# Kernel tuning notes

Measured on AMD Instinct MI355X. Metric: run time of the kernel, lower is better.

Reference implementation:

```python
import jax, jax.numpy as jnp
import numpy as np

WIN = 4
HEAD_DIM = 32
N_HEADS = 6
TYPE = 'SW'
SHIFT = WIN // 2  # window_size // 2


def _relation():
    # [P, P, 3] relative coordinate indices into the (2w-1)^3 bias table
    cord = np.array([[i, j, k] for i in range(WIN) for j in range(WIN) for k in range(WIN)])
    return cord[:, None, :] - cord[None, :, :] + WIN - 1


def _shift_mask(nw):
    # boolean mask [nw^3, P, P]; True -> -inf (cross-boundary pairs in shifted windows)
    p, s = WIN, WIN - SHIFT
    m = np.zeros((nw, nw, nw, p, p, p, p, p, p), dtype=bool)
    m[-1, :, :, :s, :, :, s:, :, :] = True
    m[-1, :, :, s:, :, :, :s, :, :] = True
    m[:, -1, :, :, :s, :, :, s:, :] = True
    m[:, -1, :, :, s:, :, :, :s, :] = True
    m[:, :, -1, :, :, :s, :, :, s:] = True
    m[:, :, -1, :, :, s:, :, :, :s] = True
    return m.reshape(nw ** 3, p ** 3, p ** 3)


def setup_inputs() -> dict:
    key = jax.random.key(0)
    ks = jax.random.split(key, 6)
    dim = N_HEADS * HEAD_DIM  # 192
    B, S = 2, 32
    x = jax.random.normal(ks[0], (B, S, S, S, dim), jnp.float32)
    W_qkv = jax.random.normal(ks[1], (dim, 3 * dim), jnp.float32) * 0.02
    b_qkv = jnp.zeros((3 * dim,), jnp.float32)
    rel_params = jax.random.normal(ks[2], (N_HEADS, 2 * WIN - 1, 2 * WIN - 1, 2 * WIN - 1), jnp.float32) * 0.02
    W_out = jax.random.normal(ks[3], (dim, dim), jnp.float32) * 0.02
    b_out = jnp.zeros((dim,), jnp.float32)
    return {"x": x, "W_qkv": W_qkv, "b_qkv": b_qkv, "rel_params": rel_params, "W_out": W_out, "b_out": b_out}


def reference(x, W_qkv, b_qkv, rel_params, W_out, b_out):
    B, H, Wd, D, C = x.shape
    p = WIN
    nw = H // p
    scale = HEAD_DIM ** -0.5
    if TYPE != 'W':
        x = jnp.roll(x, (-SHIFT, -SHIFT, -SHIFT), axis=(1, 2, 3))
    # window partition: [B, NW, P, C], NW = nw^3, P = p^3
    xw = x.reshape(B, nw, p, nw, p, nw, p, C).transpose(0, 1, 3, 5, 2, 4, 6, 7).reshape(B, nw ** 3, p ** 3, C)
    qkv = xw @ W_qkv + b_qkv  # [B, NW, P, 3C]
    qkv = qkv.reshape(B, nw ** 3, p ** 3, 3 * N_HEADS, HEAD_DIM).transpose(3, 0, 1, 2, 4)  # [3h, B, NW, P, d]
    q, k, v = qkv[:N_HEADS], qkv[N_HEADS:2 * N_HEADS], qkv[2 * N_HEADS:]
    sim = jnp.einsum('hbwpc,hbwqc->hbwpq', q, k) * scale
    rel = _relation()
    bias = rel_params[:, rel[:, :, 0], rel[:, :, 1], rel[:, :, 2]]  # [h, P, P]
    sim = sim + bias[:, None, None, :, :]
    if TYPE != 'W':
        mask = jnp.asarray(_shift_mask(nw))[None, None]  # [1,1,NW,P,P]
        sim = jnp.where(mask, -jnp.inf, sim)
    probs = jax.nn.softmax(sim, axis=-1)
    out = jnp.einsum('hbwpq,hbwqc->hbwpc', probs, v)
    out = out.transpose(1, 2, 3, 0, 4).reshape(B, nw ** 3, p ** 3, C)  # h b w p c -> b w p (h c)
    out = out @ W_out + b_out
    out = out.reshape(B, nw, nw, nw, p, p, p, C).transpose(0, 1, 4, 2, 5, 3, 6, 7).reshape(B, H, Wd, D, C)
    if TYPE != 'W':
        out = jnp.roll(out, (SHIFT, SHIFT, SHIFT), axis=(1, 2, 3))
    return out
```

## Files before the change

### kernel.cpp

```cpp
#include <hip/hip_runtime.h>

typedef short bf16x8 __attribute__((ext_vector_type(8)));
typedef float f32x4 __attribute__((ext_vector_type(4)));

#define MFMA16(a, b, c) __builtin_amdgcn_mfma_f32_16x16x32_bf16(a, b, c, 0, 0, 0)

__device__ __forceinline__ unsigned short f2bf(float f) {
    unsigned int u = __float_as_uint(f);
    u += 0x7FFFu + ((u >> 16) & 1u);
    return (unsigned short)(u >> 16);
}
__device__ __forceinline__ unsigned int f2bf2(float a, float b) {
    unsigned int ua = __float_as_uint(a);
    ua += 0x7FFFu + ((ua >> 16) & 1u);
    unsigned int ub = __float_as_uint(b);
    ub += 0x7FFFu + ((ub >> 16) & 1u);
    return (ua >> 16) | (ub & 0xFFFF0000u);
}
#define DPPADD(v, CTRL)                                                        \
    {                                                                          \
        int _t = __builtin_amdgcn_mov_dpp(__float_as_int(v), CTRL, 0xf, 0xf, true); \
        v += __int_as_float(_t);                                               \
    }

#define WQT_OFF 0
#define WOT_OFF 221184
#define BQ_OFF  294912
#define TBL_OFF 297216

__global__ void prep_kernel(const float* __restrict__ Wqkv,
                            const float* __restrict__ bqkv,
                            const float* __restrict__ Wout,
                            const float* __restrict__ rel,
                            unsigned short* __restrict__ WqT,
                            unsigned short* __restrict__ WoT,
                            float* __restrict__ bq,
                            float* __restrict__ tblB) {
    __shared__ float tile[32][33];
    const float LOG2E = 1.4426950408889634f;
    const float SCALE = 0.17677669529663687f * 1.4426950408889634f;
    int bid = blockIdx.x;
    int tx = threadIdx.x & 31, ty = threadIdx.x >> 5;
    if (bid < 108) {
        int tn = bid % 18, tc = bid / 18;
#pragma unroll
        for (int i = 0; i < 4; ++i)
            tile[ty + i * 8][tx] = Wqkv[(tc * 32 + ty + i * 8) * 576 + tn * 32 + tx];
        __syncthreads();
        bool isQ = (tn < 6);
#pragma unroll
        for (int i = 0; i < 4; ++i) {
            float v = tile[tx][ty + i * 8];
            if (isQ) v *= SCALE;
            WqT[(tn * 32 + ty + i * 8) * 192 + tc * 32 + tx] = f2bf(v);
        }
    } else if (bid < 144) {
        int bb = bid - 108;
        int tn = bb % 6, tc = bb / 6;
#pragma unroll
        for (int i = 0; i < 4; ++i)
            tile[ty + i * 8][tx] = Wout[(tc * 32 + ty + i * 8) * 192 + tn * 32 + tx];
        __syncthreads();
#pragma unroll
        for (int i = 0; i < 4; ++i)
            WoT[(tn * 32 + ty + i * 8) * 192 + tc * 32 + tx] = f2bf(tile[tx][ty + i * 8]);
    } else if (bid == 144) {
        for (int i = threadIdx.x; i < 576; i += 256) {
            float v = bqkv[i];
            if (i < 192) v *= SCALE;
            bq[i] = v;
        }
    } else {
        int e = (bid - 145) * 256 + threadIdx.x;
        int r = e & 3, f = (e >> 2) & 3;
        int lane = (e >> 4) & 63, mb = (e >> 10) & 3, h = e >> 12;
        int g = lane >> 4, l15 = lane & 15;
        int qy = l15 >> 2, qx = l15 & 3;
        int dz = mb - f + 3, dy = g - qy + 3, dx = r - qx + 3;
        tblB[e] = rel[((h * 7 + dz) * 7 + dy) * 7 + dx] * LOG2E;
    }
}

#define OFF_X   0
#define OFF_P   0
#define OFF_QK  12288
#define OFF_VT  37376
#define OFF_O   51200
#define SMEM_US 64512

__global__ __launch_bounds__(512) void wmsa_kernel(
    const float* __restrict__ x, const float* __restrict__ tblB,
    const float* __restrict__ bout,
    const unsigned short* __restrict__ WqT,
    const unsigned short* __restrict__ WoT,
    const float* __restrict__ bq, float* __restrict__ out) {
    __shared__ __align__(16) unsigned short smem[SMEM_US];

    const int tid = threadIdx.x;
    const int bw = blockIdx.x;
    const int b  = bw >> 9;
    const int w  = bw & 511;
    const int wz = w >> 6, wy = (w >> 3) & 7, wx = w & 7;

    const int lane = tid & 63;
    const int wv   = tid >> 6;
    const int g    = lane >> 4;
    const int l15  = lane & 15;

    {
        int t = tid >> 3, q8 = tid & 7;
        int tz = t >> 4, ty = (t >> 2) & 3, tx = t & 3;
        int gz = (wz * 4 + tz + 2) & 31;
        int gy = (wy * 4 + ty + 2) & 31;
        int gx = (wx * 4 + tx + 2) & 31;
        const float* xp = x + ((((b * 32 + gz) * 32 + gy) * 32 + gx)) * 192;
        int g0 = q8 >> 1, j0 = (q8 & 1) * 4, lt = t & 15;
#pragma unroll
        for (int k = 0; k < 6; ++k) {
            float4 v = *(const float4*)(xp + q8 * 4 + k * 32);
            uint2 pk;
            pk.x = f2bf2(v.x, v.y);
            pk.y = f2bf2(v.z, v.w);
            *(uint2*)&smem[OFF_X + ((((k * 4 + g0) * 4 + tz) * 16 + lt) * 8) + j0] = pk;
        }
    }

    int nb = wv;
    float bias = bq[nb * 16 + l15];
    bf16x8 bfr[6];
    {
        const unsigned short* wp = WqT + (nb * 16 + l15) * 192 + g * 8;
#pragma unroll
        for (int kk = 0; kk < 6; ++kk) bfr[kk] = *(const bf16x8*)(wp + kk * 32);
    }
    __syncthreads();

    {
        bf16x8 afr[4][6];
#pragma unroll
        for (int m = 0; m < 4; ++m)
#pragma unroll
            for (int kk = 0; kk < 6; ++kk)
                afr[m][kk] = *(const bf16x8*)&smem[OFF_X + (((kk * 4 + g) * 4 + m) * 16 + l15) * 8];

        while (true) {
            int nbN = nb + 8;
            bool more = (nbN < 36);
            bf16x8 bfrN[6];
            float biasN = 0.f;
            if (more) {
                biasN = bq[nbN * 16 + l15];
                const unsigned short* wp = WqT + (nbN * 16 + l15) * 192 + g * 8;
#pragma unroll
                for (int kk = 0; kk < 6; ++kk) bfrN[kk] = *(const bf16x8*)(wp + kk * 32);
            }
            int colg = nb * 16 + l15;
            bool isV = (nb >= 24);
#pragma unroll
            for (int m = 0; m < 4; ++m) {
                f32x4 acc = {bias, bias, bias, bias};
#pragma unroll
                for (int kk = 0; kk < 6; ++kk) acc = MFMA16(afr[m][kk], bfr[kk], acc);
                int row0 = m * 16 + g * 4;
                unsigned int u01 = f2bf2(acc[0], acc[1]);
                unsigned int u23 = f2bf2(acc[2], acc[3]);
                if (!isV) {
                    unsigned short* qk = &smem[OFF_QK + row0 * 392 + colg];
                    qk[0]    = (unsigned short)u01;
                    qk[392]  = (unsigned short)(u01 >> 16);
                    qk[784]  = (unsigned short)u23;
                    qk[1176] = (unsigned short)(u23 >> 16);
                } else {
                    uint2 pk; pk.x = u01; pk.y = u23;
                    *(uint2*)&smem[OFF_VT + (colg - 384) * 72 + row0] = pk;
                }
            }
            if (!more) break;
            nb = nbN;
            bias = biasN;
#pragma unroll
            for (int kk = 0; kk < 6; ++kk) bfr[kk] = bfrN[kk];
        }
    }
    __syncthreads();

    const bool sz = (wz == 7), sy = (wy == 7), sx = (wx == 7);
    const bool anym = sz | sy | sx;
    {
        const int qy = l15 >> 2, qx = l15 & 3;
        const bool my = sy && ((g < 2) != (qy < 2));
        bool mxr[4];
#pragma unroll
        for (int r = 0; r < 4; ++r) mxr[r] = sx && ((r < 2) != (qx < 2));
        unsigned short* pb = &smem[OFF_P + wv * 1152];
        const int it0 = wv * 3;
        int h = it0 >> 2, mb = it0 & 3;

        bf16x8 qf, kf[4];
        f32x4 bv[4];
        {
            const f32x4* tp = (const f32x4*)(tblB + ((h * 4 + mb) * 64 + lane) * 16);
#pragma unroll
            for (int f = 0; f < 4; ++f) bv[f] = tp[f];
            qf = *(const bf16x8*)&smem[OFF_QK + (mb * 16 + l15) * 392 + h * 32 + g * 8];
#pragma unroll
            for (int f = 0; f < 4; ++f)
                kf[f] = *(const bf16x8*)&smem[OFF_QK + (f * 16 + l15) * 392 + 192 + h * 32 + g * 8];
        }

#pragma unroll
        for (int ii = 0; ii < 3; ++ii) {
            bf16x8 qfN, kfN[4];
            f32x4 bvN[4];
            if (ii < 2) {
                int itN = it0 + ii + 1;
                int hN = itN >> 2, mbN = itN & 3;
                const f32x4* tp = (const f32x4*)(tblB + ((hN * 4 + mbN) * 64 + lane) * 16);
#pragma unroll
                for (int f = 0; f < 4; ++f) bvN[f] = tp[f];
                qfN = *(const bf16x8*)&smem[OFF_QK + (mbN * 16 + l15) * 392 + hN * 32 + g * 8];
#pragma unroll
                for (int f = 0; f < 4; ++f)
                    kfN[f] = *(const bf16x8*)&smem[OFF_QK + (f * 16 + l15) * 392 + 192 + hN * 32 + g * 8];
            }
            const int vtb = OFF_VT + (h * 32 + l15) * 72 + g * 8;
            bf16x8 v00 = *(const bf16x8*)&smem[vtb];
            bf16x8 v01 = *(const bf16x8*)&smem[vtb + 32];
            bf16x8 v10 = *(const bf16x8*)&smem[vtb + 16 * 72];
            bf16x8 v11 = *(const bf16x8*)&smem[vtb + 16 * 72 + 32];

            f32x4 s[4];
#pragma unroll
            for (int f = 0; f < 4; ++f) {
                f32x4 z = {0.f, 0.f, 0.f, 0.f};
                s[f] = MFMA16(qf, kf[f], z);
            }
            if (!anym) {
#pragma unroll
                for (int f = 0; f < 4; ++f)
#pragma unroll
                    for (int r = 0; r < 4; ++r)
                        s[f][r] = exp2f(s[f][r] + bv[f][r]);
            } else {
#pragma unroll
                for (int f = 0; f < 4; ++f) {
                    bool mzy = (sz && ((mb < 2) != (f < 2))) | my;
#pragma unroll
                    for (int r = 0; r < 4; ++r) {
                        float v = s[f][r] + bv[f][r];
                        v = (mzy | mxr[r]) ? -1e30f : v;
                        s[f][r] = exp2f(v);
                    }
                }
            }
            float inv[4];
#pragma unroll
            for (int r = 0; r < 4; ++r) {
                float sm = (s[0][r] + s[1][r]) + (s[2][r] + s[3][r]);
                DPPADD(sm, 0xB1);
                DPPADD(sm, 0x4E);
                DPPADD(sm, 0x124);
                DPPADD(sm, 0x128);
                inv[r] = __builtin_amdgcn_rcpf(sm);
            }
#pragma unroll
            for (int f = 0; f < 4; ++f) {
                unsigned int u01 = f2bf2(s[f][0], s[f][1]);
                unsigned int u23 = f2bf2(s[f][2], s[f][3]);
                unsigned short* pw = &pb[(g * 4) * 72 + f * 16 + l15];
                pw[0]   = (unsigned short)u01;
                pw[72]  = (unsigned short)(u01 >> 16);
                pw[144] = (unsigned short)u23;
                pw[216] = (unsigned short)(u23 >> 16);
            }
            bf16x8 pf0 = *(const bf16x8*)&pb[l15 * 72 + g * 8];
            bf16x8 pf1 = *(const bf16x8*)&pb[l15 * 72 + 32 + g * 8];
            f32x4 o0 = {0.f, 0.f, 0.f, 0.f}, o1 = {0.f, 0.f, 0.f, 0.f};
            o0 = MFMA16(pf0, v00, o0);
            o1 = MFMA16(pf0, v10, o1);
            o0 = MFMA16(pf1, v01, o0);
            o1 = MFMA16(pf1, v11, o1);
#pragma unroll
            for (int r = 0; r < 4; ++r) { o0[r] *= inv[r]; o1[r] *= inv[r]; }
            unsigned int a0 = f2bf2(o0[0], o0[1]), a1 = f2bf2(o0[2], o0[3]);
            unsigned int c0 = f2bf2(o1[0], o1[1]), c1 = f2bf2(o1[2], o1[3]);
            unsigned short* ow = &smem[OFF_O + (mb * 16 + g * 4) * 208 + h * 32 + l15];
            ow[0]        = (unsigned short)a0;
            ow[208]      = (unsigned short)(a0 >> 16);
            ow[416]      = (unsigned short)a1;
            ow[624]      = (unsigned short)(a1 >> 16);
            ow[16]       = (unsigned short)c0;
            ow[16 + 208] = (unsigned short)(c0 >> 16);
            ow[16 + 416] = (unsigned short)c1;
            ow[16 + 624] = (unsigned short)(c1 >> 16);
            if (ii < 2) {
                int itN = it0 + ii + 1;
                h = itN >> 2; mb = itN & 3;
                qf = qfN;
#pragma unroll
                for (int f = 0; f < 4; ++f) { kf[f] = kfN[f]; bv[f] = bvN[f]; }
            }
        }
    }

    const int mw = wv >> 2, nq = wv & 3;
    int col0 = nq * 16 + l15;
    float boc = bout[col0];
    bf16x8 bfr3[6];
    {
        const unsigned short* wp = WoT + col0 * 192 + g * 8;
#pragma unroll
        for (int kk = 0; kk < 6; ++kk) bfr3[kk] = *(const bf16x8*)(wp + kk * 32);
    }
    __syncthreads();

    {
        bf16x8 ofr[2][6];
#pragma unroll
        for (int mi = 0; mi < 2; ++mi)
#pragma unroll
            for (int kk = 0; kk < 6; ++kk)
                ofr[mi][kk] = *(const bf16x8*)&smem[OFF_O + ((mw * 2 + mi) * 16 + l15) * 208 + kk * 32 + g * 8];
#pragma unroll
        for (int nbi = 0; nbi < 3; ++nbi) {
            int col = (nq + nbi * 4) * 16 + l15;
            float boN = 0.f;
            bf16x8 bfrN[6];
            if (nbi < 2) {
                int colN = (nq + (nbi + 1) * 4) * 16 + l15;
                boN = bout[colN];
                const unsigned short* wp = WoT + colN * 192 + g * 8;
#pragma unroll
                for (int kk = 0; kk < 6; ++kk) bfrN[kk] = *(const bf16x8*)(wp + kk * 32);
            }
#pragma unroll
            for (int mi = 0; mi < 2; ++mi) {
                f32x4 acc = {boc, boc, boc, boc};
#pragma unroll
                for (int kk = 0; kk < 6; ++kk) acc = MFMA16(ofr[mi][kk], bfr3[kk], acc);
                int m = mw * 2 + mi;
                int gz = (wz * 4 + m + 2) & 31;
                int gy = (wy * 4 + g + 2) & 31;
#pragma unroll
                for (int r = 0; r < 4; ++r) {
                    int gx = (wx * 4 + r + 2) & 31;
                    out[(((b * 32 + gz) * 32 + gy) * 32 + gx) * 192 + col] = acc[r];
                }
            }
            boc = boN;
#pragma unroll
            for (int kk = 0; kk < 6; ++kk) bfr3[kk] = bfrN[kk];
        }
    }
}

extern "C" void kernel_launch(void* const* d_in, const int* in_sizes, int n_in,
                              void* d_out, int out_size, void* d_ws, size_t ws_size,
                              hipStream_t stream) {
    const float* x    = (const float*)d_in[0];
    const float* Wqkv = (const float*)d_in[1];
    const float* bqkv = (const float*)d_in[2];
    const float* rel  = (const float*)d_in[3];
    const float* Wout = (const float*)d_in[4];
    const float* bout = (const float*)d_in[5];

    unsigned short* WqT = (unsigned short*)((char*)d_ws + WQT_OFF);
    unsigned short* WoT = (unsigned short*)((char*)d_ws + WOT_OFF);
    float*          bq  = (float*)((char*)d_ws + BQ_OFF);
    float*          tbl = (float*)((char*)d_ws + TBL_OFF);
    float*          out = (float*)d_out;

    prep_kernel<<<241, 256, 0, stream>>>(Wqkv, bqkv, Wout, rel, WqT, WoT, bq, tbl);
    wmsa_kernel<<<1024, 512, 0, stream>>>(x, tbl, bout, WqT, WoT, bq, out);
}
```

Before: 163.2 us.

## Double block size to 1024 threads and redistribute work across 16 waves

Raises the block from 8 to 16 wavefronts and splits every stage across them. The QKV projection now gives each wave half the rows, attention uses one or two head/row-block iterations per wave, and the output projection gives each wave one row block. An extra shared-memory region holds the additional waves' probability buffers. The intent is more latency hiding and parallelism per window, at the cost of more LDS per block, fewer resident blocks per CU, and uneven work across waves in the attention stage.

New measurement: 191.4 us. +17.3%, slower.

```diff
diff --git a/kernel.cpp b/kernel.cpp
--- a/kernel.cpp
+++ b/kernel.cpp
@@ -86,9 +86,10 @@
 #define OFF_QK  12288
 #define OFF_VT  37376
 #define OFF_O   51200
-#define SMEM_US 64512
-
-__global__ __launch_bounds__(512) void wmsa_kernel(
+#define OFF_P2  64512
+#define SMEM_US 71424
+
+__global__ __launch_bounds__(1024) void wmsa_kernel(
     const float* __restrict__ x, const float* __restrict__ tblB,
     const float* __restrict__ bout,
     const unsigned short* __restrict__ WqT,
@@ -108,24 +109,26 @@
     const int l15  = lane & 15;
 
     {
-        int t = tid >> 3, q8 = tid & 7;
+        int t = tid >> 4, q16 = tid & 15;
         int tz = t >> 4, ty = (t >> 2) & 3, tx = t & 3;
         int gz = (wz * 4 + tz + 2) & 31;
         int gy = (wy * 4 + ty + 2) & 31;
         int gx = (wx * 4 + tx + 2) & 31;
         const float* xp = x + ((((b * 32 + gz) * 32 + gy) * 32 + gx)) * 192;
-        int g0 = q8 >> 1, j0 = (q8 & 1) * 4, lt = t & 15;
-#pragma unroll
-        for (int k = 0; k < 6; ++k) {
-            float4 v = *(const float4*)(xp + q8 * 4 + k * 32);
+        int g0 = (q16 >> 1) & 3, j0 = (q16 & 1) * 4, k0 = q16 >> 3, lt = t & 15;
+#pragma unroll
+        for (int k = 0; k < 3; ++k) {
+            float4 v = *(const float4*)(xp + q16 * 4 + k * 64);
             uint2 pk;
             pk.x = f2bf2(v.x, v.y);
             pk.y = f2bf2(v.z, v.w);
-            *(uint2*)&smem[OFF_X + ((((k * 4 + g0) * 4 + tz) * 16 + lt) * 8) + j0] = pk;
-        }
-    }
-
-    int nb = wv;
+            int kk = k0 + 2 * k;
+            *(uint2*)&smem[OFF_X + ((((kk * 4 + g0) * 4 + tz) * 16 + lt) * 8) + j0] = pk;
+        }
+    }
+
+    int nb = wv >> 1;
+    const int mh2 = (wv & 1) * 2;
     float bias = bq[nb * 16 + l15];
     bf16x8 bfr[6];
     {
@@ -136,12 +139,12 @@
     __syncthreads();
 
     {
-        bf16x8 afr[4][6];
-#pragma unroll
-        for (int m = 0; m < 4; ++m)
+        bf16x8 afr[2][6];
+#pragma unroll
+        for (int mi = 0; mi < 2; ++mi)
 #pragma unroll
             for (int kk = 0; kk < 6; ++kk)
-                afr[m][kk] = *(const bf16x8*)&smem[OFF_X + (((kk * 4 + g) * 4 + m) * 16 + l15) * 8];
+                afr[mi][kk] = *(const bf16x8*)&smem[OFF_X + (((kk * 4 + g) * 4 + (mh2 + mi)) * 16 + l15) * 8];
 
         while (true) {
             int nbN = nb + 8;
@@ -157,11 +160,11 @@
             int colg = nb * 16 + l15;
             bool isV = (nb >= 24);
 #pragma unroll
-            for (int m = 0; m < 4; ++m) {
+            for (int mi = 0; mi < 2; ++mi) {
                 f32x4 acc = {bias, bias, bias, bias};
 #pragma unroll
-                for (int kk = 0; kk < 6; ++kk) acc = MFMA16(afr[m][kk], bfr[kk], acc);
-                int row0 = m * 16 + g * 4;
+                for (int kk = 0; kk < 6; ++kk) acc = MFMA16(afr[mi][kk], bfr[kk], acc);
+                int row0 = (mh2 + mi) * 16 + g * 4;
                 unsigned int u01 = f2bf2(acc[0], acc[1]);
                 unsigned int u23 = f2bf2(acc[2], acc[3]);
                 if (!isV) {
@@ -192,9 +195,9 @@
         bool mxr[4];
 #pragma unroll
         for (int r = 0; r < 4; ++r) mxr[r] = sx && ((r < 2) != (qx < 2));
-        unsigned short* pb = &smem[OFF_P + wv * 1152];
-        const int it0 = wv * 3;
-        int h = it0 >> 2, mb = it0 & 3;
+        unsigned short* pb = &smem[(wv < 10) ? (OFF_P + wv * 1152) : (OFF_P2 + (wv - 10) * 1152)];
+        const int nu = (wv < 8) ? 1 : 2;
+        int h = wv >> 2, mb = wv & 3;
 
         bf16x8 qf, kf[4];
         f32x4 bv[4];
@@ -209,11 +212,13 @@
         }
 
 #pragma unroll
-        for (int ii = 0; ii < 3; ++ii) {
+        for (int ii = 0; ii < 2; ++ii) {
+            if (ii >= nu) break;
+            bool hasN = (ii + 1 < nu);
             bf16x8 qfN, kfN[4];
             f32x4 bvN[4];
-            if (ii < 2) {
-                int itN = it0 + ii + 1;
+            if (hasN) {
+                int itN = wv + 8;
                 int hN = itN >> 2, mbN = itN & 3;
                 const f32x4* tp = (const f32x4*)(tblB + ((hN * 4 + mbN) * 64 + lane) * 16);
 #pragma unroll
@@ -293,8 +298,8 @@
             ow[16 + 208] = (unsigned short)(c0 >> 16);
             ow[16 + 416] = (unsigned short)c1;
             ow[16 + 624] = (unsigned short)(c1 >> 16);
-            if (ii < 2) {
-                int itN = it0 + ii + 1;
+            if (hasN) {
+                int itN = wv + 8;
                 h = itN >> 2; mb = itN & 3;
                 qf = qfN;
 #pragma unroll
@@ -303,7 +308,7 @@
         }
     }
 
-    const int mw = wv >> 2, nq = wv & 3;
+    const int mw = wv & 3, nq = wv >> 2;
     int col0 = nq * 16 + l15;
     float boc = bout[col0];
     bf16x8 bfr3[6];
@@ -315,12 +320,13 @@
     __syncthreads();
 
     {
-        bf16x8 ofr[2][6];
-#pragma unroll
-        for (int mi = 0; mi < 2; ++mi)
-#pragma unroll
-            for (int kk = 0; kk < 6; ++kk)
-                ofr[mi][kk] = *(const bf16x8*)&smem[OFF_O + ((mw * 2 + mi) * 16 + l15) * 208 + kk * 32 + g * 8];
+        bf16x8 ofr[6];
+#pragma unroll
+        for (int kk = 0; kk < 6; ++kk)
+            ofr[kk] = *(const bf16x8*)&smem[OFF_O + (mw * 16 + l15) * 208 + kk * 32 + g * 8];
+        int gz = (wz * 4 + mw + 2) & 31;
+        int gy = (wy * 4 + g + 2) & 31;
+        float* outp = out + (((b * 32 + gz) * 32 + gy) * 32) * 192;
 #pragma unroll
         for (int nbi = 0; nbi < 3; ++nbi) {
             int col = (nq + nbi * 4) * 16 + l15;
@@ -333,19 +339,13 @@
 #pragma unroll
                 for (int kk = 0; kk < 6; ++kk) bfrN[kk] = *(const bf16x8*)(wp + kk * 32);
             }
-#pragma unroll
-            for (int mi = 0; mi < 2; ++mi) {
-                f32x4 acc = {boc, boc, boc, boc};
-#pragma unroll
-                for (int kk = 0; kk < 6; ++kk) acc = MFMA16(ofr[mi][kk], bfr3[kk], acc);
-                int m = mw * 2 + mi;
-                int gz = (wz * 4 + m + 2) & 31;
-                int gy = (wy * 4 + g + 2) & 31;
-#pragma unroll
-                for (int r = 0; r < 4; ++r) {
-                    int gx = (wx * 4 + r + 2) & 31;
-                    out[(((b * 32 + gz) * 32 + gy) * 32 + gx) * 192 + col] = acc[r];
-                }
+            f32x4 acc = {boc, boc, boc, boc};
+#pragma unroll
+            for (int kk = 0; kk < 6; ++kk) acc = MFMA16(ofr[kk], bfr3[kk], acc);
+#pragma unroll
+            for (int r = 0; r < 4; ++r) {
+                int gx = (wx * 4 + r + 2) & 31;
+                outp[gx * 192 + col] = acc[r];
             }
             boc = boN;
 #pragma unroll
@@ -371,5 +371,5 @@
     float*          out = (float*)d_out;
 
     prep_kernel<<<241, 256, 0, stream>>>(Wqkv, bqkv, Wout, rel, WqT, WoT, bq, tbl);
-    wmsa_kernel<<<1024, 512, 0, stream>>>(x, tbl, bout, WqT, WoT, bq, out);
-}
+    wmsa_kernel<<<1024, 1024, 0, stream>>>(x, tbl, bout, WqT, WoT, bq, out);
+}
```
